# Optimization experiments

Measured on AMD Instinct MI355X. Metric: run time of the kernel, lower is better.

Reference implementation:

```python
import jax, jax.numpy as jnp
import numpy as np

N, E, F, H = 50000, 800000, 128, 128
EPS = 1e-5


def _layernorm(x, gamma, beta):
    mu = jnp.mean(x, axis=-1, keepdims=True)
    var = jnp.mean(jnp.square(x - mu), axis=-1, keepdims=True)
    return (x - mu) * jax.lax.rsqrt(var + EPS) * gamma + beta


def setup_inputs() -> dict:
    key = jax.random.key(0)
    ks = jax.random.split(key, 12)
    x = jax.random.normal(ks[0], (N, F), dtype=jnp.float32)
    edge_idx = jax.random.randint(ks[1], (2, E), 0, N, dtype=jnp.int64)
    edge_attr = jax.random.normal(ks[2], (E, H), dtype=jnp.float32)
    u = jax.random.normal(ks[3], (N, H), dtype=jnp.float32)
    # node_mlp_1 params: Linear(F+H -> H), Linear(H -> H), LayerNorm(H)
    W1a = jax.random.normal(ks[4], (F + H, H), dtype=jnp.float32) / np.sqrt(F + H)
    b1a = jnp.zeros((H,), jnp.float32)
    W2a = jax.random.normal(ks[5], (H, H), dtype=jnp.float32) / np.sqrt(H)
    b2a = jnp.zeros((H,), jnp.float32)
    g1 = jnp.ones((H,), jnp.float32)
    be1 = jnp.zeros((H,), jnp.float32)
    # node_mlp_2 params: Linear(F+2H -> H), Linear(H -> H), LayerNorm(H)
    W1b = jax.random.normal(ks[6], (F + 2 * H, H), dtype=jnp.float32) / np.sqrt(F + 2 * H)
    b1b = jnp.zeros((H,), jnp.float32)
    W2b = jax.random.normal(ks[7], (H, H), dtype=jnp.float32) / np.sqrt(H)
    b2b = jnp.zeros((H,), jnp.float32)
    g2 = jnp.ones((H,), jnp.float32)
    be2 = jnp.zeros((H,), jnp.float32)
    return dict(x=x, edge_idx=edge_idx, edge_attr=edge_attr, u=u,
                W1a=W1a, b1a=b1a, W2a=W2a, b2a=b2a, g1=g1, be1=be1,
                W1b=W1b, b1b=b1b, W2b=W2b, b2b=b2b, g2=g2, be2=be2)


def reference(x, edge_idx, edge_attr, u,
              W1a, b1a, W2a, b2a, g1, be1,
              W1b, b1b, W2b, b2b, g2, be2):
    row, col = edge_idx[0], edge_idx[1]
    # gather source nodes, concat with edge features -> [E, F+H]
    msg = jnp.concatenate([x[col], edge_attr], axis=1)
    h = jax.nn.relu(msg @ W1a + b1a)
    h = _layernorm(h @ W2a + b2a, g1, be1)  # [E, H]
    # scatter_mean over destination nodes
    summed = jax.ops.segment_sum(h, row, num_segments=x.shape[0])
    counts = jax.ops.segment_sum(jnp.ones((h.shape[0],), h.dtype), row,
                                 num_segments=x.shape[0])
    agg = summed / jnp.clip(counts, 1.0)[:, None]  # [N, H]
    z = jnp.concatenate([x, agg, u], axis=1)  # [N, F+2H]
    z = jax.nn.relu(z @ W1b + b1b)
    return _layernorm(z @ W2b + b2b, g2, be2)  # [N, H]
```

## Files before the change

kernel.cpp:

```cpp
#include <hip/hip_runtime.h>


typedef __bf16 bf16x8 __attribute__((ext_vector_type(8)));
typedef float floatx4 __attribute__((ext_vector_type(4)));

__device__ __forceinline__ unsigned short f2bf(float f) {
    unsigned int u = __float_as_uint(f);
    u = u + 0x7FFFu + ((u >> 16) & 1u);
    return (unsigned short)(u >> 16);
}
__device__ __forceinline__ unsigned int pk2(float a, float b) {
    return (unsigned int)f2bf(a) | ((unsigned int)f2bf(b) << 16);
}

__global__ void detect_idx64(const unsigned int* __restrict__ idx, int* __restrict__ flag) {
    if (threadIdx.x == 0 && blockIdx.x == 0) {
        unsigned int o = 0;
        for (int i = 1; i < 64; i += 2) o |= idx[i];
        *flag = (o == 0u) ? 1 : 0;
    }
}

__global__ void prep_weights(const float* __restrict__ W1a, const float* __restrict__ W2a,
                             const float* __restrict__ W1b, const float* __restrict__ W2b,
                             unsigned short* __restrict__ w1aT, unsigned short* __restrict__ w2aT,
                             unsigned short* __restrict__ w1bT, unsigned short* __restrict__ w2bT) {
    int g = blockIdx.x * 256 + threadIdx.x;
    if (g < 32768) {
        int n = g >> 8, k = g & 255;
        w1aT[g] = f2bf(W1a[k * 128 + n]);
    } else if (g < 49152) {
        int l = g - 32768; int n = l >> 7, k = l & 127;
        w2aT[l] = f2bf(W2a[k * 128 + n]);
    } else if (g < 98304) {
        int l = g - 49152; int n = l / 384, k = l - n * 384;
        w1bT[l] = f2bf(W1b[k * 128 + n]);
    } else if (g < 114688) {
        int l = g - 98304; int n = l >> 7, k = l & 127;
        w2bT[l] = f2bf(W2b[k * 128 + n]);
    }
}

__global__ __launch_bounds__(256, 2) void edge_mlp_scatter(
    const float* __restrict__ x, const void* __restrict__ eidx,
    const float* __restrict__ ea,
    const float* __restrict__ b1a, const float* __restrict__ b2a,
    const float* __restrict__ g1, const float* __restrict__ be1,
    const unsigned short* __restrict__ w1aT, const unsigned short* __restrict__ w2aT,
    float* __restrict__ summed, float* __restrict__ counts,
    const int* __restrict__ flag64, int E)
{
    __shared__ union {
        unsigned short msg[64 * 264];
        float h2[64 * 132];
    } uA;
    __shared__ unsigned short h1s[64 * 136];
    __shared__ int lsRow[64], lsCol[64];
    __shared__ float sMean[64], sRstd[64];

    const int tid  = threadIdx.x;
    const int lane = tid & 63;
    const int wave = tid >> 6;
    const int quad = lane >> 4;
    const int lm   = lane & 15;
    const int ns   = wave * 32;

    bf16x8 wf1[8][2], wf2[4][2];
#pragma unroll
    for (int kk = 0; kk < 8; kk++)
#pragma unroll
        for (int nt = 0; nt < 2; nt++)
            wf1[kk][nt] = *(const bf16x8*)(w1aT + (ns + nt * 16 + lm) * 256 + kk * 32 + quad * 8);
#pragma unroll
    for (int kk = 0; kk < 4; kk++)
#pragma unroll
        for (int nt = 0; nt < 2; nt++)
            wf2[kk][nt] = *(const bf16x8*)(w2aT + (ns + nt * 16 + lm) * 128 + kk * 32 + quad * 8);

    float b1v[2], b2v[2];
#pragma unroll
    for (int nt = 0; nt < 2; nt++) {
        b1v[nt] = b1a[ns + nt * 16 + lm];
        b2v[nt] = b2a[ns + nt * 16 + lm];
    }
    const int colT = tid & 127;
    const float gv = g1[colT], bev = be1[colT];
    const int use64 = *flag64;

    const int numTiles = (E + 63) >> 6;
    for (int t = blockIdx.x; t < numTiles; t += gridDim.x) {
        const int eb = t << 6;
        __syncthreads();
        if (tid < 64) {
            int e = eb + tid; if (e >= E) e = E - 1;
            int r, c;
            if (use64) { const long long* p = (const long long*)eidx; r = (int)p[e]; c = (int)p[E + e]; }
            else       { const int* p = (const int*)eidx;             r = p[e];      c = p[E + e]; }
            lsRow[tid] = r; lsCol[tid] = c;
        }
        __syncthreads();
        {
            const int rl = tid >> 5, l32 = tid & 31;
#pragma unroll
            for (int it = 0; it < 8; it++) {
                const int e = it * 8 + rl;
                int eg = eb + e; if (eg >= E) eg = E - 1;
                const float4 xv = ((const float4*)(x + (size_t)lsCol[e] * 128))[l32];
                const float4 av = ((const float4*)(ea + (size_t)eg * 128))[l32];
                *(unsigned int*)&uA.msg[e * 264 + l32 * 4]           = pk2(xv.x, xv.y);
                *(unsigned int*)&uA.msg[e * 264 + l32 * 4 + 2]       = pk2(xv.z, xv.w);
                *(unsigned int*)&uA.msg[e * 264 + 128 + l32 * 4]     = pk2(av.x, av.y);
                *(unsigned int*)&uA.msg[e * 264 + 128 + l32 * 4 + 2] = pk2(av.z, av.w);
            }
        }
        __syncthreads();
        floatx4 acc1[4][2] = {};
#pragma unroll
        for (int mt = 0; mt < 4; mt++)
#pragma unroll
            for (int kk = 0; kk < 8; kk++) {
                bf16x8 a = *(const bf16x8*)&uA.msg[(mt * 16 + lm) * 264 + kk * 32 + quad * 8];
                acc1[mt][0] = __builtin_amdgcn_mfma_f32_16x16x32_bf16(a, wf1[kk][0], acc1[mt][0], 0, 0, 0);
                acc1[mt][1] = __builtin_amdgcn_mfma_f32_16x16x32_bf16(a, wf1[kk][1], acc1[mt][1], 0, 0, 0);
            }
#pragma unroll
        for (int mt = 0; mt < 4; mt++)
#pragma unroll
            for (int nt = 0; nt < 2; nt++)
#pragma unroll
                for (int r = 0; r < 4; r++) {
                    const int row = mt * 16 + quad * 4 + r;
                    const int col = ns + nt * 16 + lm;
                    h1s[row * 136 + col] = f2bf(fmaxf(acc1[mt][nt][r] + b1v[nt], 0.f));
                }
        __syncthreads();
        floatx4 acc2[4][2] = {};
#pragma unroll
        for (int mt = 0; mt < 4; mt++)
#pragma unroll
            for (int kk = 0; kk < 4; kk++) {
                bf16x8 a = *(const bf16x8*)&h1s[(mt * 16 + lm) * 136 + kk * 32 + quad * 8];
                acc2[mt][0] = __builtin_amdgcn_mfma_f32_16x16x32_bf16(a, wf2[kk][0], acc2[mt][0], 0, 0, 0);
                acc2[mt][1] = __builtin_amdgcn_mfma_f32_16x16x32_bf16(a, wf2[kk][1], acc2[mt][1], 0, 0, 0);
            }
#pragma unroll
        for (int mt = 0; mt < 4; mt++)
#pragma unroll
            for (int nt = 0; nt < 2; nt++)
#pragma unroll
                for (int r = 0; r < 4; r++) {
                    const int row = mt * 16 + quad * 4 + r;
                    const int col = ns + nt * 16 + lm;
                    uA.h2[row * 132 + col] = acc2[mt][nt][r] + b2v[nt];
                }
        __syncthreads();
        {
            const int e = tid >> 2, q = tid & 3;
            const float4* hp = (const float4*)&uA.h2[e * 132 + q * 32];
            float s = 0.f, ss = 0.f;
#pragma unroll
            for (int i = 0; i < 8; i++) {
                float4 v = hp[i];
                s  += v.x + v.y + v.z + v.w;
                ss += v.x * v.x + v.y * v.y + v.z * v.z + v.w * v.w;
            }
            s  += __shfl_xor(s, 1);  s  += __shfl_xor(s, 2);
            ss += __shfl_xor(ss, 1); ss += __shfl_xor(ss, 2);
            if (q == 0) {
                float mean = s * (1.f / 128.f);
                float var  = ss * (1.f / 128.f) - mean * mean;
                sMean[e] = mean;
                sRstd[e] = rsqrtf(var + 1e-5f);
                if (eb + e < E) atomicAdd(counts + lsRow[e], 1.f);
            }
        }
        __syncthreads();
        {
            const int half = tid >> 7;
#pragma unroll
            for (int it = 0; it < 32; it++) {
                const int e = it * 2 + half;
                if (eb + e < E) {
                    float v = (uA.h2[e * 132 + colT] - sMean[e]) * sRstd[e] * gv + bev;
                    atomicAdd(summed + (size_t)lsRow[e] * 128 + colT, v);
                }
            }
        }
    }
}

__global__ __launch_bounds__(256, 2) void node_mlp(
    const float* __restrict__ x, const float* __restrict__ u,
    const float* summed, const float* __restrict__ counts,
    const float* __restrict__ b1b, const float* __restrict__ b2b,
    const float* __restrict__ g2, const float* __restrict__ be2,
    const unsigned short* __restrict__ w1bT, const unsigned short* __restrict__ w2bT,
    float* out, int NN)
{
    __shared__ union {
        unsigned short msg[32 * 392];
        float h2[32 * 132];
    } uA;
    __shared__ unsigned short h1s[32 * 136];
    __shared__ float sMean[32], sRstd[32];

    const int tid  = threadIdx.x;
    const int lane = tid & 63;
    const int wave = tid >> 6;
    const int quad = lane >> 4;
    const int lm   = lane & 15;
    const int ns   = wave * 32;

    bf16x8 wf1[12][2], wf2[4][2];
#pragma unroll
    for (int kk = 0; kk < 12; kk++)
#pragma unroll
        for (int nt = 0; nt < 2; nt++)
            wf1[kk][nt] = *(const bf16x8*)(w1bT + (ns + nt * 16 + lm) * 384 + kk * 32 + quad * 8);
#pragma unroll
    for (int kk = 0; kk < 4; kk++)
#pragma unroll
        for (int nt = 0; nt < 2; nt++)
            wf2[kk][nt] = *(const bf16x8*)(w2bT + (ns + nt * 16 + lm) * 128 + kk * 32 + quad * 8);

    float b1v[2], b2v[2];
#pragma unroll
    for (int nt = 0; nt < 2; nt++) {
        b1v[nt] = b1b[ns + nt * 16 + lm];
        b2v[nt] = b2b[ns + nt * 16 + lm];
    }
    const int colT = tid & 127;
    const float gv = g2[colT], bev = be2[colT];

    const int numTiles = (NN + 31) >> 5;
    for (int t = blockIdx.x; t < numTiles; t += gridDim.x) {
        const int nb = t << 5;
        __syncthreads();
        {
            const int rl = tid >> 5, l32 = tid & 31;
#pragma unroll
            for (int it = 0; it < 4; it++) {
                const int rloc = it * 8 + rl;
                int i = nb + rloc; if (i >= NN) i = NN - 1;
                const float4 xv = ((const float4*)(x + (size_t)i * 128))[l32];
                float4 sv = ((const float4*)(summed + (size_t)i * 128))[l32];
                const float inv = 1.f / fmaxf(counts[i], 1.f);
                sv.x *= inv; sv.y *= inv; sv.z *= inv; sv.w *= inv;
                const float4 uv = ((const float4*)(u + (size_t)i * 128))[l32];
                *(unsigned int*)&uA.msg[rloc * 392 + l32 * 4]           = pk2(xv.x, xv.y);
                *(unsigned int*)&uA.msg[rloc * 392 + l32 * 4 + 2]       = pk2(xv.z, xv.w);
                *(unsigned int*)&uA.msg[rloc * 392 + 128 + l32 * 4]     = pk2(sv.x, sv.y);
                *(unsigned int*)&uA.msg[rloc * 392 + 128 + l32 * 4 + 2] = pk2(sv.z, sv.w);
                *(unsigned int*)&uA.msg[rloc * 392 + 256 + l32 * 4]     = pk2(uv.x, uv.y);
                *(unsigned int*)&uA.msg[rloc * 392 + 256 + l32 * 4 + 2] = pk2(uv.z, uv.w);
            }
        }
        __syncthreads();
        floatx4 acc1[2][2] = {};
#pragma unroll
        for (int mt = 0; mt < 2; mt++)
#pragma unroll
            for (int kk = 0; kk < 12; kk++) {
                bf16x8 a = *(const bf16x8*)&uA.msg[(mt * 16 + lm) * 392 + kk * 32 + quad * 8];
                acc1[mt][0] = __builtin_amdgcn_mfma_f32_16x16x32_bf16(a, wf1[kk][0], acc1[mt][0], 0, 0, 0);
                acc1[mt][1] = __builtin_amdgcn_mfma_f32_16x16x32_bf16(a, wf1[kk][1], acc1[mt][1], 0, 0, 0);
            }
#pragma unroll
        for (int mt = 0; mt < 2; mt++)
#pragma unroll
            for (int nt = 0; nt < 2; nt++)
#pragma unroll
                for (int r = 0; r < 4; r++) {
                    const int row = mt * 16 + quad * 4 + r;
                    const int col = ns + nt * 16 + lm;
                    h1s[row * 136 + col] = f2bf(fmaxf(acc1[mt][nt][r] + b1v[nt], 0.f));
                }
        __syncthreads();
        floatx4 acc2[2][2] = {};
#pragma unroll
        for (int mt = 0; mt < 2; mt++)
#pragma unroll
            for (int kk = 0; kk < 4; kk++) {
                bf16x8 a = *(const bf16x8*)&h1s[(mt * 16 + lm) * 136 + kk * 32 + quad * 8];
                acc2[mt][0] = __builtin_amdgcn_mfma_f32_16x16x32_bf16(a, wf2[kk][0], acc2[mt][0], 0, 0, 0);
                acc2[mt][1] = __builtin_amdgcn_mfma_f32_16x16x32_bf16(a, wf2[kk][1], acc2[mt][1], 0, 0, 0);
            }
#pragma unroll
        for (int mt = 0; mt < 2; mt++)
#pragma unroll
            for (int nt = 0; nt < 2; nt++)
#pragma unroll
                for (int r = 0; r < 4; r++) {
                    const int row = mt * 16 + quad * 4 + r;
                    const int col = ns + nt * 16 + lm;
                    uA.h2[row * 132 + col] = acc2[mt][nt][r] + b2v[nt];
                }
        __syncthreads();
        {
            const int e = tid >> 3, q = tid & 7;
            const float4* hp = (const float4*)&uA.h2[e * 132 + q * 16];
            float s = 0.f, ss = 0.f;
#pragma unroll
            for (int i = 0; i < 4; i++) {
                float4 v = hp[i];
                s  += v.x + v.y + v.z + v.w;
                ss += v.x * v.x + v.y * v.y + v.z * v.z + v.w * v.w;
            }
            s  += __shfl_xor(s, 1);  s  += __shfl_xor(s, 2);  s  += __shfl_xor(s, 4);
            ss += __shfl_xor(ss, 1); ss += __shfl_xor(ss, 2); ss += __shfl_xor(ss, 4);
            if (q == 0) {
                float mean = s * (1.f / 128.f);
                float var  = ss * (1.f / 128.f) - mean * mean;
                sMean[e] = mean;
                sRstd[e] = rsqrtf(var + 1e-5f);
            }
        }
        __syncthreads();
        {
            const int half = tid >> 7;
#pragma unroll
            for (int it = 0; it < 16; it++) {
                const int rloc = it * 2 + half;
                const int i = nb + rloc;
                if (i < NN) {
                    float v = (uA.h2[rloc * 132 + colT] - sMean[rloc]) * sRstd[rloc] * gv + bev;
                    out[(size_t)i * 128 + colT] = v;
                }
            }
        }
    }
}

extern "C" void kernel_launch(void* const* d_in, const int* in_sizes, int n_in,
                              void* d_out, int out_size, void* d_ws, size_t ws_size,
                              hipStream_t stream)
{
    const float* x   = (const float*)d_in[0];
    const void*  eidx = d_in[1];
    const float* ea  = (const float*)d_in[2];
    const float* u   = (const float*)d_in[3];
    const float* W1a = (const float*)d_in[4];
    const float* b1a = (const float*)d_in[5];
    const float* W2a = (const float*)d_in[6];
    const float* b2a = (const float*)d_in[7];
    const float* g1  = (const float*)d_in[8];
    const float* be1 = (const float*)d_in[9];
    const float* W1b = (const float*)d_in[10];
    const float* b1b = (const float*)d_in[11];
    const float* W2b = (const float*)d_in[12];
    const float* b2b = (const float*)d_in[13];
    const float* g2  = (const float*)d_in[14];
    const float* be2 = (const float*)d_in[15];

    const int NN = in_sizes[0] / 128;
    const int E  = in_sizes[2] / 128;

    float* counts = (float*)d_ws;
    int*   flag   = (int*)((char*)d_ws + (size_t)NN * 4);
    size_t woff   = (((size_t)NN * 4 + 4) + 15) & ~(size_t)15;
    unsigned short* w1aT = (unsigned short*)((char*)d_ws + woff);
    unsigned short* w2aT = w1aT + 128 * 256;
    unsigned short* w1bT = w2aT + 128 * 128;
    unsigned short* w2bT = w1bT + 128 * 384;

    float* outf = (float*)d_out;

    hipMemsetAsync(d_out, 0, (size_t)out_size * 4, stream);
    hipMemsetAsync(counts, 0, (size_t)NN * 4, stream);
    detect_idx64<<<1, 64, 0, stream>>>((const unsigned int*)eidx, flag);
    prep_weights<<<448, 256, 0, stream>>>(W1a, W2a, W1b, W2b, w1aT, w2aT, w1bT, w2bT);

    edge_mlp_scatter<<<512, 256, 0, stream>>>(x, eidx, ea, b1a, b2a, g1, be1,
                                              w1aT, w2aT, outf, counts, flag, E);

    const int nodeTiles = (NN + 31) >> 5;
    node_mlp<<<nodeTiles, 256, 0, stream>>>(x, u, outf, counts, b1b, b2b, g2, be2,
                                            w1bT, w2bT, outf, NN);
}
```

Baseline: 964.1 us.

## Accumulate scatter-mean sums in packed fp16 with unsafe hardware atomics

The scatter of edge-MLP outputs now uses packed half2 atomic adds into a workspace fp16 buffer when the workspace is large enough, which halves atomic traffic and the number of atomic operations. All float atomics switch to unsafeAtomicAdd so the hardware float atomic instructions can be used. The node kernel reads the fp16 sums and launches a fixed 512-block persistent grid. fp16 accumulation of about 16 values per node adds rounding error and overflow risk relative to fp32 sums.

```diff
diff --git a/kernel.cpp b/kernel.cpp
--- a/kernel.cpp
+++ b/kernel.cpp
@@ -1,4 +1,5 @@
 #include <hip/hip_runtime.h>
+#include <hip/hip_fp16.h>
 
 
 typedef __bf16 bf16x8 __attribute__((ext_vector_type(8)));
@@ -47,8 +48,9 @@
     const float* __restrict__ b1a, const float* __restrict__ b2a,
     const float* __restrict__ g1, const float* __restrict__ be1,
     const unsigned short* __restrict__ w1aT, const unsigned short* __restrict__ w2aT,
-    float* __restrict__ summed, float* __restrict__ counts,
-    const int* __restrict__ flag64, int E)
+    float* __restrict__ summed, __half* __restrict__ summedH,
+    float* __restrict__ counts,
+    const int* __restrict__ flag64, int E, int useHalf)
 {
     __shared__ union {
         unsigned short msg[64 * 264];
@@ -85,6 +87,12 @@
     }
     const int colT = tid & 127;
     const float gv = g1[colT], bev = be1[colT];
+    const int colP = tid & 63, eg4 = tid >> 6;
+    float gA = 0.f, gB = 0.f, bA = 0.f, bB = 0.f;
+    if (useHalf) {
+        gA = g1[colP * 2];  gB = g1[colP * 2 + 1];
+        bA = be1[colP * 2]; bB = be1[colP * 2 + 1];
+    }
     const int use64 = *flag64;
 
     const int numTiles = (E + 63) >> 6;
@@ -171,18 +179,30 @@
                 float var  = ss * (1.f / 128.f) - mean * mean;
                 sMean[e] = mean;
                 sRstd[e] = rsqrtf(var + 1e-5f);
-                if (eb + e < E) atomicAdd(counts + lsRow[e], 1.f);
-            }
-        }
-        __syncthreads();
-        {
-            const int half = tid >> 7;
+                if (eb + e < E) unsafeAtomicAdd(counts + lsRow[e], 1.f);
+            }
+        }
+        __syncthreads();
+        if (useHalf) {
+#pragma unroll
+            for (int it = 0; it < 16; it++) {
+                const int e = it * 4 + eg4;
+                if (eb + e < E) {
+                    const float2 h = *(const float2*)&uA.h2[e * 132 + colP * 2];
+                    const float m = sMean[e], rs = sRstd[e];
+                    const float v0 = (h.x - m) * rs * gA + bA;
+                    const float v1 = (h.y - m) * rs * gB + bB;
+                    unsafeAtomicAdd((__half2*)(summedH + (size_t)lsRow[e] * 128 + colP * 2),
+                                    __floats2half2_rn(v0, v1));
+                }
+            }
+        } else {
 #pragma unroll
             for (int it = 0; it < 32; it++) {
-                const int e = it * 2 + half;
+                const int e = it * 2 + (tid >> 7);
                 if (eb + e < E) {
                     float v = (uA.h2[e * 132 + colT] - sMean[e]) * sRstd[e] * gv + bev;
-                    atomicAdd(summed + (size_t)lsRow[e] * 128 + colT, v);
+                    unsafeAtomicAdd(summed + (size_t)lsRow[e] * 128 + colT, v);
                 }
             }
         }
@@ -191,11 +211,12 @@
 
 __global__ __launch_bounds__(256, 2) void node_mlp(
     const float* __restrict__ x, const float* __restrict__ u,
-    const float* summed, const float* __restrict__ counts,
+    const float* summed, const __half* __restrict__ summedH,
+    const float* __restrict__ counts,
     const float* __restrict__ b1b, const float* __restrict__ b2b,
     const float* __restrict__ g2, const float* __restrict__ be2,
     const unsigned short* __restrict__ w1bT, const unsigned short* __restrict__ w2bT,
-    float* out, int NN)
+    float* out, int NN, int useHalf)
 {
     __shared__ union {
         unsigned short msg[32 * 392];
@@ -243,7 +264,17 @@
                 const int rloc = it * 8 + rl;
                 int i = nb + rloc; if (i >= NN) i = NN - 1;
                 const float4 xv = ((const float4*)(x + (size_t)i * 128))[l32];
-                float4 sv = ((const float4*)(summed + (size_t)i * 128))[l32];
+                float4 sv;
+                if (useHalf) {
+                    const float2 rw = ((const float2*)(summedH + (size_t)i * 128))[l32];
+                    const __half2 h01 = *(const __half2*)&rw.x;
+                    const __half2 h23 = *(const __half2*)&rw.y;
+                    const float2 a = __half22float2(h01);
+                    const float2 b = __half22float2(h23);
+                    sv.x = a.x; sv.y = a.y; sv.z = b.x; sv.w = b.y;
+                } else {
+                    sv = ((const float4*)(summed + (size_t)i * 128))[l32];
+                }
                 const float inv = 1.f / fmaxf(counts[i], 1.f);
                 sv.x *= inv; sv.y *= inv; sv.z *= inv; sv.w *= inv;
                 const float4 uv = ((const float4*)(u + (size_t)i * 128))[l32];
@@ -362,18 +393,24 @@
     unsigned short* w2aT = w1aT + 128 * 256;
     unsigned short* w1bT = w2aT + 128 * 128;
     unsigned short* w2bT = w1bT + 128 * 384;
+    size_t shoff  = (woff + (size_t)(128*256 + 128*128 + 128*384 + 128*128) * 2 + 255) & ~(size_t)255;
+    __half* summedH = (__half*)((char*)d_ws + shoff);
+    const int useHalf = (ws_size >= shoff + (size_t)NN * 128 * 2) ? 1 : 0;
 
     float* outf = (float*)d_out;
 
-    hipMemsetAsync(d_out, 0, (size_t)out_size * 4, stream);
+    if (useHalf) {
+        hipMemsetAsync(summedH, 0, (size_t)NN * 128 * 2, stream);
+    } else {
+        hipMemsetAsync(d_out, 0, (size_t)out_size * 4, stream);
+    }
     hipMemsetAsync(counts, 0, (size_t)NN * 4, stream);
     detect_idx64<<<1, 64, 0, stream>>>((const unsigned int*)eidx, flag);
     prep_weights<<<448, 256, 0, stream>>>(W1a, W2a, W1b, W2b, w1aT, w2aT, w1bT, w2bT);
 
     edge_mlp_scatter<<<512, 256, 0, stream>>>(x, eidx, ea, b1a, b2a, g1, be1,
-                                              w1aT, w2aT, outf, counts, flag, E);
-
-    const int nodeTiles = (NN + 31) >> 5;
-    node_mlp<<<nodeTiles, 256, 0, stream>>>(x, u, outf, counts, b1b, b2b, g2, be2,
-                                            w1bT, w2bT, outf, NN);
-}
+                                              w1aT, w2aT, outf, summedH, counts, flag, E, useHalf);
+
+    node_mlp<<<512, 256, 0, stream>>>(x, u, outf, summedH, counts, b1b, b2b, g2, be2,
+                                      w1bT, w2bT, outf, NN, useHalf);
+}
```

After: 795.6 us. 17.5% less time.
